# Kernel tuning notes

Measured on AMD Instinct MI355X. Metric: run time of the kernel, lower is better.

## Reference

```python
import jax, jax.numpy as jnp
import numpy as np

RRELU_SLOPE = 0.2  # eval-mode RReLU with lower=0.1, upper=0.3 -> (0.1+0.3)/2


def setup_inputs() -> dict:
    key = jax.random.key(0)
    k1, k2, k3 = jax.random.split(key, 3)
    B, C, H, W = 16, 64, 256, 256
    x = jax.random.normal(k1, (B, C, H, W), dtype=jnp.float32)
    mix = jax.random.normal(k2, (C, C), dtype=jnp.float32) / np.sqrt(C)
    bias = jax.random.normal(k3, (C,), dtype=jnp.float32) * 0.1
    return {"x": x, "mix": mix, "bias": bias}


def reference(x, mix, bias):
    # Softmax2d: softmax over channel dim at each spatial location
    s = jax.nn.softmax(x, axis=1)                     # (B,C,H,W)
    # channel mix: out[d] = sum_c mix[d,c] * s[c]  (== s_flat @ mix.T in torch)
    mixed = jnp.einsum('bchw,dc->bdhw', s, mix)
    mixed = mixed + bias[None, :, None, None]
    # RReLU (deterministic eval-mode slope)
    activated = jnp.where(mixed >= 0, mixed, RRELU_SLOPE * mixed)
    out = jax.nn.relu(activated + 0.1 * x)
    return out
```

## Files before the change

kernel.cpp:

```cpp
#include <hip/hip_runtime.h>
#include <math.h>

#define HWSZ 65536

typedef __bf16 bf16x8 __attribute__((ext_vector_type(8)));
typedef __bf16 bf16x4 __attribute__((ext_vector_type(4)));
typedef float f32x4 __attribute__((ext_vector_type(4)));

__global__ __launch_bounds__(256) void cvt_mix_kernel(const float* __restrict__ mix,
                                                      __bf16* __restrict__ mixb) {
    int i = blockIdx.x * 256 + threadIdx.x;
    mixb[i] = (__bf16)mix[i];
}

__global__ __launch_bounds__(256, 5) void fused_kernel(
    const float* __restrict__ x, const __bf16* __restrict__ mixb,
    const float* __restrict__ bias, float* __restrict__ out)
{
    __shared__ __bf16 sT[4][64 * 64];
    const int tid  = threadIdx.x;
    const int wid  = tid >> 6;
    const int lane = tid & 63;
    const int waveg = blockIdx.x * 4 + wid;
    const int b   = waveg >> 10;
    const int hw0 = (waveg & 1023) << 6;
    const size_t ibase = (size_t)b * (64 * HWSZ) + hw0;

    const float LOG2E = 1.44269504088896340736f;
    const float LN2   = 0.69314718055994530942f;

    const float* xp = x + ibase + lane;
    float e[64];
#pragma unroll
    for (int c = 0; c < 64; ++c) e[c] = xp[(size_t)c << 16];

    float m0 = e[0], m1 = e[1], m2 = e[2], m3 = e[3];
#pragma unroll
    for (int c = 4; c < 64; c += 4) {
        m0 = fmaxf(m0, e[c]);     m1 = fmaxf(m1, e[c + 1]);
        m2 = fmaxf(m2, e[c + 2]); m3 = fmaxf(m3, e[c + 3]);
    }
    const float m = fmaxf(fmaxf(m0, m1), fmaxf(m2, m3));

    float s0 = 0.f, s1 = 0.f, s2 = 0.f, s3 = 0.f;
#pragma unroll
    for (int c = 0; c < 64; c += 4) {
        e[c]     = __builtin_exp2f((e[c]     - m) * LOG2E); s0 += e[c];
        e[c + 1] = __builtin_exp2f((e[c + 1] - m) * LOG2E); s1 += e[c + 1];
        e[c + 2] = __builtin_exp2f((e[c + 2] - m) * LOG2E); s2 += e[c + 2];
        e[c + 3] = __builtin_exp2f((e[c + 3] - m) * LOG2E); s3 += e[c + 3];
    }
    const float sum = (s0 + s1) + (s2 + s3);
    const float inv = 1.f / sum;
    const float Mv = fmaf(LN2, __builtin_log2f(sum), m);

    __bf16* my = &sT[wid][0];
#pragma unroll
    for (int j = 0; j < 8; ++j) {
        bf16x8 v;
#pragma unroll
        for (int i = 0; i < 8; ++i) v[i] = (__bf16)(e[j * 8 + i] * inv);
        const int gr = j ^ (lane & 7);
        *reinterpret_cast<bf16x8*>(my + lane * 64 + gr * 8) = v;
    }
    asm volatile("s_waitcnt lgkmcnt(0)" ::: "memory");

    const int l15 = lane & 15, lhi = lane >> 4;

    float Mp[4];
#pragma unroll
    for (int nt = 0; nt < 4; ++nt)
        Mp[nt] = __shfl(Mv, nt * 16 + l15, 64);

#pragma unroll
    for (int mtp = 0; mtp < 2; ++mtp) {
        f32x4 acc[2][4] = {};
#pragma unroll
        for (int kt = 0; kt < 2; ++kt) {
            bf16x8 A[2], B[4];
            const __bf16* ab = mixb + (mtp * 32 + l15) * 64 + kt * 32 + lhi * 8;
#pragma unroll
            for (int mt = 0; mt < 2; ++mt)
                A[mt] = *reinterpret_cast<const bf16x8*>(ab + mt * 16 * 64);
#pragma unroll
            for (int nt = 0; nt < 4; ++nt) {
                const int row = nt * 16 + l15;
                const int g = (kt * 4 + lhi) ^ (row & 7);
                B[nt] = *reinterpret_cast<const bf16x8*>(my + row * 64 + g * 8);
            }
#pragma unroll
            for (int mt = 0; mt < 2; ++mt)
#pragma unroll
                for (int nt = 0; nt < 4; ++nt)
                    acc[mt][nt] = __builtin_amdgcn_mfma_f32_16x16x32_bf16(
                        A[mt], B[nt], acc[mt][nt], 0, 0, 0);
        }

#pragma unroll
        for (int mt = 0; mt < 2; ++mt) {
            const int d0 = mtp * 32 + mt * 16 + lhi * 4;
            const float bb[4] = {bias[d0], bias[d0 + 1], bias[d0 + 2], bias[d0 + 3]};
#pragma unroll
            for (int nt = 0; nt < 4; ++nt) {
                const int p = nt * 16 + l15;
                const int g = ((d0 >> 3) ^ (p & 7));
                const bf16x4 sv = *reinterpret_cast<const bf16x4*>(
                    my + p * 64 + g * 8 + (d0 & 7));
                float* orw = out + ibase + (size_t)d0 * HWSZ + p;
#pragma unroll
                for (int r = 0; r < 4; ++r) {
                    float mixed = acc[mt][nt][r] + bb[r];
                    float act = fmaxf(mixed, 0.2f * mixed);
                    float xv = fmaf(LN2, __builtin_log2f((float)sv[r]), Mp[nt]);
                    float v = fmaf(0.1f, xv, act);
                    orw[(size_t)r * HWSZ] = fmaxf(v, 0.f);
                }
            }
        }
    }
}

extern "C" void kernel_launch(void* const* d_in, const int* in_sizes, int n_in,
                              void* d_out, int out_size, void* d_ws, size_t ws_size,
                              hipStream_t stream) {
    const float* x    = (const float*)d_in[0];
    const float* mix  = (const float*)d_in[1];
    const float* bias = (const float*)d_in[2];
    float* out = (float*)d_out;
    __bf16* mixb = (__bf16*)d_ws;
    (void)in_sizes; (void)n_in; (void)out_size; (void)ws_size;

    cvt_mix_kernel<<<dim3(16), dim3(256), 0, stream>>>(mix, mixb);
    fused_kernel<<<dim3(4096), dim3(256), 0, stream>>>(x, mixb, bias, out);
}
```

Measured before the change: 119.7 us.

## Process two pixel tiles per wave and prefetch second tile during MFMA

Each wave now handles two consecutive 64-pixel tiles instead of one, and the grid is halved. The second tile's global loads are issued right after the first tile's softmax, so they are in flight while the first tile's MFMA and epilogue run. This hides memory latency within a wave rather than relying only on occupancy. Launch bounds drop from 5 to 3 waves per SIMD to make room for the extra registers, which lowers occupancy. The MFMA loop is also reordered so B fragments are consumed as soon as they are loaded.

```diff
diff --git a/kernel.cpp b/kernel.cpp
--- a/kernel.cpp
+++ b/kernel.cpp
@@ -13,27 +13,9 @@
     mixb[i] = (__bf16)mix[i];
 }
 
-__global__ __launch_bounds__(256, 5) void fused_kernel(
-    const float* __restrict__ x, const __bf16* __restrict__ mixb,
-    const float* __restrict__ bias, float* __restrict__ out)
-{
-    __shared__ __bf16 sT[4][64 * 64];
-    const int tid  = threadIdx.x;
-    const int wid  = tid >> 6;
-    const int lane = tid & 63;
-    const int waveg = blockIdx.x * 4 + wid;
-    const int b   = waveg >> 10;
-    const int hw0 = (waveg & 1023) << 6;
-    const size_t ibase = (size_t)b * (64 * HWSZ) + hw0;
-
+__device__ __forceinline__ float softmax_to_lds(float (&e)[64], __bf16* my, int lane) {
     const float LOG2E = 1.44269504088896340736f;
     const float LN2   = 0.69314718055994530942f;
-
-    const float* xp = x + ibase + lane;
-    float e[64];
-#pragma unroll
-    for (int c = 0; c < 64; ++c) e[c] = xp[(size_t)c << 16];
-
     float m0 = e[0], m1 = e[1], m2 = e[2], m3 = e[3];
 #pragma unroll
     for (int c = 4; c < 64; c += 4) {
@@ -41,7 +23,6 @@
         m2 = fmaxf(m2, e[c + 2]); m3 = fmaxf(m3, e[c + 3]);
     }
     const float m = fmaxf(fmaxf(m0, m1), fmaxf(m2, m3));
-
     float s0 = 0.f, s1 = 0.f, s2 = 0.f, s3 = 0.f;
 #pragma unroll
     for (int c = 0; c < 64; c += 4) {
@@ -52,9 +33,6 @@
     }
     const float sum = (s0 + s1) + (s2 + s3);
     const float inv = 1.f / sum;
-    const float Mv = fmaf(LN2, __builtin_log2f(sum), m);
-
-    __bf16* my = &sT[wid][0];
 #pragma unroll
     for (int j = 0; j < 8; ++j) {
         bf16x8 v;
@@ -63,39 +41,30 @@
         const int gr = j ^ (lane & 7);
         *reinterpret_cast<bf16x8*>(my + lane * 64 + gr * 8) = v;
     }
-    asm volatile("s_waitcnt lgkmcnt(0)" ::: "memory");
+    return fmaf(LN2, __builtin_log2f(sum), m);
+}
 
-    const int l15 = lane & 15, lhi = lane >> 4;
-
-    float Mp[4];
-#pragma unroll
-    for (int nt = 0; nt < 4; ++nt)
-        Mp[nt] = __shfl(Mv, nt * 16 + l15, 64);
-
+__device__ __forceinline__ void mfma_epilogue(const __bf16* my, const __bf16* mixb,
+                                              const float* bias, float* ob,
+                                              const float (&Mp)[4], int l15, int lhi) {
+    const float LN2 = 0.69314718055994530942f;
 #pragma unroll
     for (int mtp = 0; mtp < 2; ++mtp) {
         f32x4 acc[2][4] = {};
 #pragma unroll
         for (int kt = 0; kt < 2; ++kt) {
-            bf16x8 A[2], B[4];
             const __bf16* ab = mixb + (mtp * 32 + l15) * 64 + kt * 32 + lhi * 8;
-#pragma unroll
-            for (int mt = 0; mt < 2; ++mt)
-                A[mt] = *reinterpret_cast<const bf16x8*>(ab + mt * 16 * 64);
+            const bf16x8 A0 = *reinterpret_cast<const bf16x8*>(ab);
+            const bf16x8 A1 = *reinterpret_cast<const bf16x8*>(ab + 16 * 64);
 #pragma unroll
             for (int nt = 0; nt < 4; ++nt) {
                 const int row = nt * 16 + l15;
                 const int g = (kt * 4 + lhi) ^ (row & 7);
-                B[nt] = *reinterpret_cast<const bf16x8*>(my + row * 64 + g * 8);
+                const bf16x8 B = *reinterpret_cast<const bf16x8*>(my + row * 64 + g * 8);
+                acc[0][nt] = __builtin_amdgcn_mfma_f32_16x16x32_bf16(A0, B, acc[0][nt], 0, 0, 0);
+                acc[1][nt] = __builtin_amdgcn_mfma_f32_16x16x32_bf16(A1, B, acc[1][nt], 0, 0, 0);
             }
-#pragma unroll
-            for (int mt = 0; mt < 2; ++mt)
-#pragma unroll
-                for (int nt = 0; nt < 4; ++nt)
-                    acc[mt][nt] = __builtin_amdgcn_mfma_f32_16x16x32_bf16(
-                        A[mt], B[nt], acc[mt][nt], 0, 0, 0);
         }
-
 #pragma unroll
         for (int mt = 0; mt < 2; ++mt) {
             const int d0 = mtp * 32 + mt * 16 + lhi * 4;
@@ -106,7 +75,7 @@
                 const int g = ((d0 >> 3) ^ (p & 7));
                 const bf16x4 sv = *reinterpret_cast<const bf16x4*>(
                     my + p * 64 + g * 8 + (d0 & 7));
-                float* orw = out + ibase + (size_t)d0 * HWSZ + p;
+                float* orw = ob + (size_t)d0 * HWSZ + p;
 #pragma unroll
                 for (int r = 0; r < 4; ++r) {
                     float mixed = acc[mt][nt][r] + bb[r];
@@ -120,6 +89,42 @@
     }
 }
 
+__global__ __launch_bounds__(256, 3) void fused_kernel(
+    const float* __restrict__ x, const __bf16* __restrict__ mixb,
+    const float* __restrict__ bias, float* __restrict__ out)
+{
+    __shared__ __bf16 sT[4][64 * 64];
+    const int tid = threadIdx.x, wid = tid >> 6, lane = tid & 63;
+    const int w = blockIdx.x * 4 + wid;
+    const int gp0 = w << 7;
+    const int b = gp0 >> 16;
+    const int hw0 = gp0 & (HWSZ - 1);
+    const size_t ibase0 = (size_t)b * (64 * HWSZ) + hw0;
+    __bf16* my = &sT[wid][0];
+    const int l15 = lane & 15, lhi = lane >> 4;
+
+    float e[64];
+    const float* xp0 = x + ibase0 + lane;
+#pragma unroll
+    for (int c = 0; c < 64; ++c) e[c] = xp0[(size_t)c << 16];
+
+    float Mv = softmax_to_lds(e, my, lane);
+    const float* xp1 = xp0 + 64;
+#pragma unroll
+    for (int c = 0; c < 64; ++c) e[c] = xp1[(size_t)c << 16];
+    asm volatile("s_waitcnt lgkmcnt(0)" ::: "memory");
+    float Mp[4];
+#pragma unroll
+    for (int nt = 0; nt < 4; ++nt) Mp[nt] = __shfl(Mv, nt * 16 + l15, 64);
+    mfma_epilogue(my, mixb, bias, out + ibase0, Mp, l15, lhi);
+
+    Mv = softmax_to_lds(e, my, lane);
+    asm volatile("s_waitcnt lgkmcnt(0)" ::: "memory");
+#pragma unroll
+    for (int nt = 0; nt < 4; ++nt) Mp[nt] = __shfl(Mv, nt * 16 + l15, 64);
+    mfma_epilogue(my, mixb, bias, out + ibase0 + 64, Mp, l15, lhi);
+}
+
 extern "C" void kernel_launch(void* const* d_in, const int* in_sizes, int n_in,
                               void* d_out, int out_size, void* d_ws, size_t ws_size,
                               hipStream_t stream) {
@@ -131,5 +136,5 @@
     (void)in_sizes; (void)n_in; (void)out_size; (void)ws_size;
 
     cvt_mix_kernel<<<dim3(16), dim3(256), 0, stream>>>(mix, mixb);
-    fused_kernel<<<dim3(4096), dim3(256), 0, stream>>>(x, mixb, bias, out);
+    fused_kernel<<<dim3(2048), dim3(256), 0, stream>>>(x, mixb, bias, out);
 }
```

Measured after the change: 226.7 us. +89.5%, slower.

## Process four pixel tiles per wave and defer softmax normalization past the MFMA

Applied to the files above, without the earlier changes.

Each wave now loops over four 64-pixel tiles, and the grid shrinks from 4096 to 1024 blocks. Unnormalized exponentials are stored to LDS, and the reciprocal sum is applied in the epilogue FMA after the matrix multiply. The per-element normalize multiply before the bf16 conversion goes away. The x reconstruction now uses log of the unnormalized bf16 exp plus the max rather than the log-sum. Fewer blocks and a serial loop may reduce latency hiding, since each wave's loads no longer overlap across tiles.

```diff
diff --git a/kernel.cpp b/kernel.cpp
--- a/kernel.cpp
+++ b/kernel.cpp
@@ -21,99 +21,97 @@
     const int tid  = threadIdx.x;
     const int wid  = tid >> 6;
     const int lane = tid & 63;
-    const int waveg = blockIdx.x * 4 + wid;
-    const int b   = waveg >> 10;
-    const int hw0 = (waveg & 1023) << 6;
-    const size_t ibase = (size_t)b * (64 * HWSZ) + hw0;
+    const int w = blockIdx.x * 4 + wid;
+    const size_t gp0 = (size_t)w << 8;
+    const int b   = (int)(gp0 >> 16);
+    const int hw0 = (int)(gp0 & (HWSZ - 1));
+    const size_t ibase = (size_t)b * ((size_t)64 * HWSZ) + hw0;
+    __bf16* my = &sT[wid][0];
+    const int l15 = lane & 15, lhi = lane >> 4;
 
     const float LOG2E = 1.44269504088896340736f;
     const float LN2   = 0.69314718055994530942f;
 
-    const float* xp = x + ibase + lane;
-    float e[64];
+#pragma unroll 1
+    for (int t = 0; t < 4; ++t) {
+        const float* xp = x + ibase + t * 64 + lane;
+        float* ob = out + ibase + t * 64;
+
+        float e[64];
 #pragma unroll
-    for (int c = 0; c < 64; ++c) e[c] = xp[(size_t)c << 16];
+        for (int c = 0; c < 64; ++c) e[c] = xp[(size_t)c << 16];
 
-    float m0 = e[0], m1 = e[1], m2 = e[2], m3 = e[3];
+        float m0 = e[0], m1 = e[1], m2 = e[2], m3 = e[3];
 #pragma unroll
-    for (int c = 4; c < 64; c += 4) {
-        m0 = fmaxf(m0, e[c]);     m1 = fmaxf(m1, e[c + 1]);
-        m2 = fmaxf(m2, e[c + 2]); m3 = fmaxf(m3, e[c + 3]);
-    }
-    const float m = fmaxf(fmaxf(m0, m1), fmaxf(m2, m3));
+        for (int c = 4; c < 64; c += 4) {
+            m0 = fmaxf(m0, e[c]);     m1 = fmaxf(m1, e[c + 1]);
+            m2 = fmaxf(m2, e[c + 2]); m3 = fmaxf(m3, e[c + 3]);
+        }
+        const float m = fmaxf(fmaxf(m0, m1), fmaxf(m2, m3));
 
-    float s0 = 0.f, s1 = 0.f, s2 = 0.f, s3 = 0.f;
+        float s0 = 0.f, s1 = 0.f, s2 = 0.f, s3 = 0.f;
 #pragma unroll
-    for (int c = 0; c < 64; c += 4) {
-        e[c]     = __builtin_exp2f((e[c]     - m) * LOG2E); s0 += e[c];
-        e[c + 1] = __builtin_exp2f((e[c + 1] - m) * LOG2E); s1 += e[c + 1];
-        e[c + 2] = __builtin_exp2f((e[c + 2] - m) * LOG2E); s2 += e[c + 2];
-        e[c + 3] = __builtin_exp2f((e[c + 3] - m) * LOG2E); s3 += e[c + 3];
-    }
-    const float sum = (s0 + s1) + (s2 + s3);
-    const float inv = 1.f / sum;
-    const float Mv = fmaf(LN2, __builtin_log2f(sum), m);
-
-    __bf16* my = &sT[wid][0];
-#pragma unroll
-    for (int j = 0; j < 8; ++j) {
-        bf16x8 v;
-#pragma unroll
-        for (int i = 0; i < 8; ++i) v[i] = (__bf16)(e[j * 8 + i] * inv);
-        const int gr = j ^ (lane & 7);
-        *reinterpret_cast<bf16x8*>(my + lane * 64 + gr * 8) = v;
-    }
-    asm volatile("s_waitcnt lgkmcnt(0)" ::: "memory");
-
-    const int l15 = lane & 15, lhi = lane >> 4;
-
-    float Mp[4];
-#pragma unroll
-    for (int nt = 0; nt < 4; ++nt)
-        Mp[nt] = __shfl(Mv, nt * 16 + l15, 64);
+        for (int c = 0; c < 64; c += 4) {
+            e[c]     = __builtin_exp2f((e[c]     - m) * LOG2E); s0 += e[c];
+            e[c + 1] = __builtin_exp2f((e[c + 1] - m) * LOG2E); s1 += e[c + 1];
+            e[c + 2] = __builtin_exp2f((e[c + 2] - m) * LOG2E); s2 += e[c + 2];
+            e[c + 3] = __builtin_exp2f((e[c + 3] - m) * LOG2E); s3 += e[c + 3];
+        }
+        const float inv = 1.f / ((s0 + s1) + (s2 + s3));
 
 #pragma unroll
-    for (int mtp = 0; mtp < 2; ++mtp) {
-        f32x4 acc[2][4] = {};
+        for (int j = 0; j < 8; ++j) {
+            bf16x8 v;
 #pragma unroll
-        for (int kt = 0; kt < 2; ++kt) {
-            bf16x8 A[2], B[4];
-            const __bf16* ab = mixb + (mtp * 32 + l15) * 64 + kt * 32 + lhi * 8;
+            for (int i = 0; i < 8; ++i) v[i] = (__bf16)e[j * 8 + i];
+            const int gr = j ^ (lane & 7);
+            *reinterpret_cast<bf16x8*>(my + lane * 64 + gr * 8) = v;
+        }
+        asm volatile("s_waitcnt lgkmcnt(0)" ::: "memory");
+
+        float mp[4], ivp[4];
 #pragma unroll
-            for (int mt = 0; mt < 2; ++mt)
-                A[mt] = *reinterpret_cast<const bf16x8*>(ab + mt * 16 * 64);
-#pragma unroll
-            for (int nt = 0; nt < 4; ++nt) {
-                const int row = nt * 16 + l15;
-                const int g = (kt * 4 + lhi) ^ (row & 7);
-                B[nt] = *reinterpret_cast<const bf16x8*>(my + row * 64 + g * 8);
-            }
-#pragma unroll
-            for (int mt = 0; mt < 2; ++mt)
-#pragma unroll
-                for (int nt = 0; nt < 4; ++nt)
-                    acc[mt][nt] = __builtin_amdgcn_mfma_f32_16x16x32_bf16(
-                        A[mt], B[nt], acc[mt][nt], 0, 0, 0);
+        for (int nt = 0; nt < 4; ++nt) {
+            mp[nt]  = __shfl(m,   nt * 16 + l15, 64);
+            ivp[nt] = __shfl(inv, nt * 16 + l15, 64);
         }
 
 #pragma unroll
-        for (int mt = 0; mt < 2; ++mt) {
-            const int d0 = mtp * 32 + mt * 16 + lhi * 4;
-            const float bb[4] = {bias[d0], bias[d0 + 1], bias[d0 + 2], bias[d0 + 3]};
+        for (int mtp = 0; mtp < 2; ++mtp) {
+            f32x4 acc[2][4] = {};
 #pragma unroll
-            for (int nt = 0; nt < 4; ++nt) {
-                const int p = nt * 16 + l15;
-                const int g = ((d0 >> 3) ^ (p & 7));
-                const bf16x4 sv = *reinterpret_cast<const bf16x4*>(
-                    my + p * 64 + g * 8 + (d0 & 7));
-                float* orw = out + ibase + (size_t)d0 * HWSZ + p;
+            for (int kt = 0; kt < 2; ++kt) {
+                const __bf16* ab = mixb + (mtp * 32 + l15) * 64 + kt * 32 + lhi * 8;
+                const bf16x8 A0 = *reinterpret_cast<const bf16x8*>(ab);
+                const bf16x8 A1 = *reinterpret_cast<const bf16x8*>(ab + 16 * 64);
 #pragma unroll
-                for (int r = 0; r < 4; ++r) {
-                    float mixed = acc[mt][nt][r] + bb[r];
-                    float act = fmaxf(mixed, 0.2f * mixed);
-                    float xv = fmaf(LN2, __builtin_log2f((float)sv[r]), Mp[nt]);
-                    float v = fmaf(0.1f, xv, act);
-                    orw[(size_t)r * HWSZ] = fmaxf(v, 0.f);
+                for (int nt = 0; nt < 4; ++nt) {
+                    const int row = nt * 16 + l15;
+                    const int g = (kt * 4 + lhi) ^ (row & 7);
+                    const bf16x8 B = *reinterpret_cast<const bf16x8*>(my + row * 64 + g * 8);
+                    acc[0][nt] = __builtin_amdgcn_mfma_f32_16x16x32_bf16(A0, B, acc[0][nt], 0, 0, 0);
+                    acc[1][nt] = __builtin_amdgcn_mfma_f32_16x16x32_bf16(A1, B, acc[1][nt], 0, 0, 0);
+                }
+            }
+#pragma unroll
+            for (int mt = 0; mt < 2; ++mt) {
+                const int d0 = mtp * 32 + mt * 16 + lhi * 4;
+                const float bb[4] = {bias[d0], bias[d0 + 1], bias[d0 + 2], bias[d0 + 3]};
+#pragma unroll
+                for (int nt = 0; nt < 4; ++nt) {
+                    const int p = nt * 16 + l15;
+                    const int g = ((d0 >> 3) ^ (p & 7));
+                    const bf16x4 sv = *reinterpret_cast<const bf16x4*>(
+                        my + p * 64 + g * 8 + (d0 & 7));
+                    float* orw = ob + (size_t)d0 * HWSZ + p;
+#pragma unroll
+                    for (int r = 0; r < 4; ++r) {
+                        float mixed = fmaf(acc[mt][nt][r], ivp[nt], bb[r]);
+                        float act = fmaxf(mixed, 0.2f * mixed);
+                        float xv = fmaf(LN2, __builtin_log2f((float)sv[r]), mp[nt]);
+                        float v = fmaf(0.1f, xv, act);
+                        orw[(size_t)r * HWSZ] = fmaxf(v, 0.f);
+                    }
                 }
             }
         }
@@ -131,5 +129,5 @@
     (void)in_sizes; (void)n_in; (void)out_size; (void)ws_size;
 
     cvt_mix_kernel<<<dim3(16), dim3(256), 0, stream>>>(mix, mixb);
-    fused_kernel<<<dim3(4096), dim3(256), 0, stream>>>(x, mixb, bias, out);
+    fused_kernel<<<dim3(1024), dim3(256), 0, stream>>>(x, mixb, bias, out);
 }
```

Result: slower. 181.1 us (+51.3%).
